# Kernel optimization log

Measured on AMD Instinct MI355X. Metric: run time of the kernel, lower is better.

The kernel has to match this reference:

```python
import jax, jax.numpy as jnp
import numpy as np

NEG_SLOPE = 0.2


def gat_layer(x, W, att_src, att_dst, bias, src, dst, N):
    # x: [N, Din], W: [Din, H*C], att_src/att_dst: [H, C], bias: [H*C]
    H, C = att_src.shape
    h = (x @ W).reshape(N, H, C)                       # [N, H, C]
    a_s = jnp.einsum('nhc,hc->nh', h, att_src)          # [N, H]
    a_d = jnp.einsum('nhc,hc->nh', h, att_dst)          # [N, H]
    e = jax.nn.leaky_relu(a_s[src] + a_d[dst], NEG_SLOPE)  # [E, H]
    # segment softmax over incoming edges of each destination node
    m = jax.ops.segment_max(e, dst, num_segments=N)     # [N, H]
    p = jnp.exp(e - m[dst])                             # [E, H]
    denom = jax.ops.segment_sum(p, dst, num_segments=N)  # [N, H]
    alpha = p / denom[dst]                              # [E, H]
    msg = alpha[:, :, None] * h[src]                    # [E, H, C]
    out = jax.ops.segment_sum(msg, dst, num_segments=N)  # [N, H, C]
    return out.reshape(N, H * C) + bias


def setup_inputs() -> dict:
    key = jax.random.key(0)
    N, E, D, H, C = 50000, 1600000, 128, 4, 32
    ks = jax.random.split(key, 12)
    x = jax.random.normal(ks[0], (N, D), dtype=jnp.float32)
    edge_index = jax.random.randint(ks[1], (2, E), 0, N, dtype=jnp.int64)
    s1 = 1.0 / np.sqrt(D)
    W1 = jax.random.normal(ks[2], (D, H * C), dtype=jnp.float32) * s1
    att_src1 = jax.random.normal(ks[3], (H, C), dtype=jnp.float32) * (1.0 / np.sqrt(C))
    att_dst1 = jax.random.normal(ks[4], (H, C), dtype=jnp.float32) * (1.0 / np.sqrt(C))
    bias1 = jnp.zeros((H * C,), dtype=jnp.float32)
    s2 = 1.0 / np.sqrt(H * C)
    W2 = jax.random.normal(ks[5], (H * C, 1), dtype=jnp.float32) * s2
    att_src2 = jax.random.normal(ks[6], (1, 1), dtype=jnp.float32)
    att_dst2 = jax.random.normal(ks[7], (1, 1), dtype=jnp.float32)
    bias2 = jnp.zeros((1,), dtype=jnp.float32)
    return {
        'x': x, 'edge_index': edge_index,
        'W1': W1, 'att_src1': att_src1, 'att_dst1': att_dst1, 'bias1': bias1,
        'W2': W2, 'att_src2': att_src2, 'att_dst2': att_dst2, 'bias2': bias2,
    }


def reference(x, edge_index, W1, att_src1, att_dst1, bias1, W2, att_src2, att_dst2, bias2):
    N = x.shape[0]
    # PyG GATConv default: add self-loops
    loop = jnp.arange(N, dtype=edge_index.dtype)
    src = jnp.concatenate([edge_index[0], loop])
    dst = jnp.concatenate([edge_index[1], loop])
    # dropout(p=0.5) is identity in eval mode
    h = gat_layer(x, W1, att_src1, att_dst1, bias1, src, dst, N)   # [N, H*C]
    h = jax.nn.elu(h)
    out = gat_layer(h, W2, att_src2, att_dst2, bias2, src, dst, N)  # [N, 1]
    return out.squeeze(-1)  # [N]
```

## Files before the change

### kernel.cpp

```cpp
#include <hip/hip_runtime.h>
#include <hip/hip_fp16.h>
#include <stdint.h>

#define NEG_SLOPE 0.2f
#define BSHIFT 7
#define NB 256

__device__ __forceinline__ float lrelu(float x){ return x > 0.f ? x : NEG_SLOPE * x; }
__device__ __forceinline__ float elu1(float x){ return x > 0.f ? x : expm1f(x); }
__device__ __forceinline__ unsigned fenc(float f){
  unsigned u = __float_as_uint(f);
  return (u & 0x80000000u) ? ~u : (u | 0x80000000u);
}
__device__ __forceinline__ float fdec(unsigned u){
  return (u & 0x80000000u) ? __uint_as_float(u & 0x7fffffffu) : __uint_as_float(~u);
}

__global__ __launch_bounds__(256) void k_gemm1(
    const float* __restrict__ x, const float* __restrict__ W1,
    const float* __restrict__ atts, const float* __restrict__ attd,
    __half* __restrict__ h1, float* __restrict__ as1, float* __restrict__ ad1,
    float* __restrict__ gblkmax, int N){
  __shared__ float xs[128 * 128];
  int n0 = blockIdx.x * 128;
  int t = threadIdx.x;
  {
    int row = t & 127;
    int kc = t >> 7;
    int n = n0 + row;
    const float4* x4 = (const float4*)x;
    #pragma unroll 4
    for (int i = 0; i < 16; ++i){
      float4 v = (n < N) ? x4[(size_t)n * 32 + kc * 16 + i]
                         : make_float4(0.f, 0.f, 0.f, 0.f);
      int k = kc * 64 + 4 * i;
      xs[(k + 0) * 128 + row] = v.x;
      xs[(k + 1) * 128 + row] = v.y;
      xs[(k + 2) * 128 + row] = v.z;
      xs[(k + 3) * 128 + row] = v.w;
    }
  }
  __syncthreads();
  int m = t & 15;
  int rg = t >> 4;
  int rb = rg * 8;
  const float4* W14 = (const float4*)W1;
  float acc[8][8];
  #pragma unroll
  for (int r = 0; r < 8; ++r)
    #pragma unroll
    for (int c = 0; c < 8; ++c) acc[r][c] = 0.f;
  #pragma unroll 2
  for (int k = 0; k < 128; ++k){
    float4 w0 = W14[k * 32 + 2 * m];
    float4 w1 = W14[k * 32 + 2 * m + 1];
    float4 xa = *(const float4*)&xs[k * 128 + rb];
    float4 xb = *(const float4*)&xs[k * 128 + rb + 4];
    float xr[8] = {xa.x, xa.y, xa.z, xa.w, xb.x, xb.y, xb.z, xb.w};
    float wc[8] = {w0.x, w0.y, w0.z, w0.w, w1.x, w1.y, w1.z, w1.w};
    #pragma unroll
    for (int r = 0; r < 8; ++r)
      #pragma unroll
      for (int c = 0; c < 8; ++c)
        acc[r][c] = fmaf(xr[r], wc[c], acc[r][c]);
  }
  float4 av0 = ((const float4*)atts)[2 * m], av1 = ((const float4*)atts)[2 * m + 1];
  float4 dv0 = ((const float4*)attd)[2 * m], dv1 = ((const float4*)attd)[2 * m + 1];
  int h = m >> 2;
  float lmax = -INFINITY;
  #pragma unroll
  for (int r = 0; r < 8; ++r){
    int n = n0 + rb + r;
    if (n < N){
      union { __half2 hh[4]; float4 f; } u;
      u.hh[0] = __floats2half2_rn(acc[r][0], acc[r][1]);
      u.hh[1] = __floats2half2_rn(acc[r][2], acc[r][3]);
      u.hh[2] = __floats2half2_rn(acc[r][4], acc[r][5]);
      u.hh[3] = __floats2half2_rn(acc[r][6], acc[r][7]);
      *(float4*)(h1 + (size_t)n * 128 + 8 * m) = u.f;
    }
    float s  = acc[r][0]*av0.x + acc[r][1]*av0.y + acc[r][2]*av0.z + acc[r][3]*av0.w
             + acc[r][4]*av1.x + acc[r][5]*av1.y + acc[r][6]*av1.z + acc[r][7]*av1.w;
    float dd = acc[r][0]*dv0.x + acc[r][1]*dv0.y + acc[r][2]*dv0.z + acc[r][3]*dv0.w
             + acc[r][4]*dv1.x + acc[r][5]*dv1.y + acc[r][6]*dv1.z + acc[r][7]*dv1.w;
    s  += __shfl_down(s, 1);  s  += __shfl_down(s, 2);
    dd += __shfl_down(dd, 1); dd += __shfl_down(dd, 2);
    lmax = fmaxf(lmax, s);
    if ((m & 3) == 0 && n < N){
      as1[n * 4 + h] = s;
      ad1[n * 4 + h] = dd;
    }
  }
  __syncthreads();
  if ((m & 3) == 0) xs[(m >> 2) * 16 + rg] = lmax;
  __syncthreads();
  if (t < 4){
    float mx = xs[t * 16];
    #pragma unroll
    for (int i = 1; i < 16; ++i) mx = fmaxf(mx, xs[t * 16 + i]);
    gblkmax[blockIdx.x * 4 + t] = mx;
  }
}


__global__ void k_bhist(const int* __restrict__ ei, int* __restrict__ gcnt,
                        int E, int N, int B, int chunk){
  __shared__ int hist[512];
  for (int t = threadIdx.x; t < B; t += 256) hist[t] = 0;
  __syncthreads();
  int T = E + N;
  int lo = blockIdx.x * chunk;
  int hi = min(lo + chunk, T);
  for (int i = lo + (int)threadIdx.x; i < hi; i += 256){
    int d = (i < E) ? ei[E + i] : (i - E);
    atomicAdd(&hist[d >> BSHIFT], 1);
  }
  __syncthreads();
  for (int t = threadIdx.x; t < B; t += 256) gcnt[blockIdx.x * B + t] = hist[t];
}

__global__ void k_bprefix(const int* __restrict__ gcnt, int* __restrict__ ecur,
                          int* __restrict__ btot, int B){
  int b = blockIdx.x;
  int t = threadIdx.x;
  int v = gcnt[t * B + b];
  int lane = t & 63, wid = t >> 6;
  int x = v;
  #pragma unroll
  for (int off = 1; off < 64; off <<= 1){
    int tmp = __shfl_up(x, off, 64);
    if (lane >= off) x += tmp;
  }
  __shared__ int ws[4];
  if (lane == 63) ws[wid] = x;
  __syncthreads();
  if (t == 0){
    int s = 0;
    #pragma unroll
    for (int i = 0; i < 4; ++i){ int tmp = ws[i]; ws[i] = s; s += tmp; }
  }
  __syncthreads();
  int excl = ws[wid] + x - v;
  ecur[b * NB + t] = excl;
  if (t == 255) btot[b] = excl + v;
}

__global__ void k_btscan(const int* __restrict__ btot, int* __restrict__ bstart,
                         const float* __restrict__ gblkmax, float* __restrict__ asmaxf,
                         unsigned* __restrict__ h2mm, int B, int T){
  __shared__ int wsum[16];
  __shared__ int carry_s;
  __shared__ unsigned smenc[4];
  int lane = threadIdx.x & 63, wid = threadIdx.x >> 6;
  if (threadIdx.x == 0) carry_s = 0;
  if (threadIdx.x < 4) smenc[threadIdx.x] = 0u;
  __syncthreads();
  for (int base = 0; base < B; base += 1024){
    int i = base + (int)threadIdx.x;
    int v = (i < B) ? btot[i] : 0;
    int x = v;
    #pragma unroll
    for (int off = 1; off < 64; off <<= 1){
      int t = __shfl_up(x, off, 64);
      if (lane >= off) x += t;
    }
    if (lane == 63) wsum[wid] = x;
    __syncthreads();
    if (wid == 0 && lane < 16){
      int w = wsum[lane];
      #pragma unroll
      for (int off = 1; off < 16; off <<= 1){
        int t = __shfl_up(w, off, 64);
        if (lane >= off) w += t;
      }
      wsum[lane] = w;
    }
    __syncthreads();
    int carry = carry_s;
    int prefix = carry + (wid ? wsum[wid - 1] : 0);
    if (i < B) bstart[i] = prefix + x - v;
    __syncthreads();
    if (threadIdx.x == 1023) carry_s = carry + wsum[15];
    __syncthreads();
  }
  if (threadIdx.x == 0) bstart[B] = T;
  float lmax = -INFINITY;
  for (int i = threadIdx.x; i < B * 4; i += 1024) lmax = fmaxf(lmax, gblkmax[i]);
  atomicMax(&smenc[threadIdx.x & 3], fenc(lmax));
  __syncthreads();
  if (threadIdx.x < 4) asmaxf[threadIdx.x] = fdec(smenc[threadIdx.x]);
  if (threadIdx.x < 2) h2mm[threadIdx.x] = 0u;
}

__global__ void k_bscatter(const int* __restrict__ ei, const int* __restrict__ ecur,
                           const int* __restrict__ bstart,
                           unsigned* __restrict__ ebuf,
                           int E, int N, int B, int chunk){
  __shared__ int cur[512];
  for (int t = threadIdx.x; t < B; t += 256)
    cur[t] = ecur[t * NB + blockIdx.x] + bstart[t];
  __syncthreads();
  int T = E + N;
  int lo = blockIdx.x * chunk;
  int hi = min(lo + chunk, T);
  for (int i = lo + (int)threadIdx.x; i < hi; i += 256){
    int s, d;
    if (i < E){ s = ei[i]; d = ei[E + i]; } else { s = d = i - E; }
    int pos = atomicAdd(&cur[d >> BSHIFT], 1);
    ebuf[pos] = ((unsigned)(d & 127) << 25) | (unsigned)s;
  }
}

__global__ void k_bfinal(const unsigned* __restrict__ ebuf,
                         const int* __restrict__ bstart,
                         int* __restrict__ csr, int* __restrict__ rs,
                         int N, int B, int T){
  int b = blockIdx.x;
  int d0 = b << BSHIFT;
  int dcount = min(128, N - d0);
  int ebeg = bstart[b];
  int eend = bstart[b + 1];
  __shared__ int hist[128];
  __shared__ int excl[128];
  if (threadIdx.x < 128) hist[threadIdx.x] = 0;
  __syncthreads();
  for (int i = ebeg + (int)threadIdx.x; i < eend; i += 256)
    atomicAdd(&hist[ebuf[i] >> 25], 1);
  __syncthreads();
  if (threadIdx.x < 64){
    int l = threadIdx.x;
    int v0 = hist[l], v1 = hist[l + 64];
    int s0 = v0, s1 = v1;
    #pragma unroll
    for (int off = 1; off < 64; off <<= 1){
      int t0 = __shfl_up(s0, off, 64); if (l >= off) s0 += t0;
      int t1 = __shfl_up(s1, off, 64); if (l >= off) s1 += t1;
    }
    int tot0 = __shfl(s0, 63, 64);
    excl[l] = s0 - v0;
    excl[l + 64] = tot0 + s1 - v1;
  }
  __syncthreads();
  if (threadIdx.x < dcount) rs[d0 + threadIdx.x] = ebeg + excl[threadIdx.x];
  if (threadIdx.x < 128) hist[threadIdx.x] = excl[threadIdx.x];
  if (b == 0 && threadIdx.x == 255) rs[N] = T;
  __syncthreads();
  for (int i = ebeg + (int)threadIdx.x; i < eend; i += 256){
    unsigned e = ebuf[i];
    int pos = ebeg + atomicAdd(&hist[e >> 25], 1);
    csr[pos] = (int)(e & 0x01FFFFFFu);
  }
}

__global__ void k_agg1(const int* __restrict__ csr, const int* __restrict__ rs,
                       const float* __restrict__ as1, const float* __restrict__ ad1,
                       const float* __restrict__ asmaxf,
                       const float4* __restrict__ h1,
                       const float* __restrict__ bias1,
                       const float* __restrict__ W2, float* __restrict__ h2, int N){
  int wv = threadIdx.x >> 6;
  int lane = threadIdx.x & 63;
  int d = blockIdx.x * 4 + wv;
  if (d >= N) return;
  int g = lane >> 4;
  int m = lane & 15;
  int h = m >> 2;
  float adh = ad1[d * 4 + h];
  float M = lrelu(asmaxf[h] + adh);
  int beg = rs[d], end = rs[d + 1];
  float den = 0.f;
  float a0=0.f,a1=0.f,a2=0.f,a3=0.f,a4=0.f,a5=0.f,a6=0.f,a7=0.f;
  int j = beg;
  for (; j + 8 <= end; j += 8){
    int sA = csr[j + g];
    int sB = csr[j + 4 + g];
    float eA = lrelu(as1[sA * 4 + h] + adh);
    float eB = lrelu(as1[sB * 4 + h] + adh);
    float pA = __expf(eA - M);
    float pB = __expf(eB - M);
    float4 rA = h1[(size_t)sA * 16 + m];
    float4 rB = h1[(size_t)sB * 16 + m];
    den += pA + pB;
    float2 cA0 = __half22float2(*(__half2*)&rA.x);
    float2 cA1 = __half22float2(*(__half2*)&rA.y);
    float2 cA2 = __half22float2(*(__half2*)&rA.z);
    float2 cA3 = __half22float2(*(__half2*)&rA.w);
    a0 = fmaf(pA, cA0.x, a0); a1 = fmaf(pA, cA0.y, a1);
    a2 = fmaf(pA, cA1.x, a2); a3 = fmaf(pA, cA1.y, a3);
    a4 = fmaf(pA, cA2.x, a4); a5 = fmaf(pA, cA2.y, a5);
    a6 = fmaf(pA, cA3.x, a6); a7 = fmaf(pA, cA3.y, a7);
    float2 cB0 = __half22float2(*(__half2*)&rB.x);
    float2 cB1 = __half22float2(*(__half2*)&rB.y);
    float2 cB2 = __half22float2(*(__half2*)&rB.z);
    float2 cB3 = __half22float2(*(__half2*)&rB.w);
    a0 = fmaf(pB, cB0.x, a0); a1 = fmaf(pB, cB0.y, a1);
    a2 = fmaf(pB, cB1.x, a2); a3 = fmaf(pB, cB1.y, a3);
    a4 = fmaf(pB, cB2.x, a4); a5 = fmaf(pB, cB2.y, a5);
    a6 = fmaf(pB, cB3.x, a6); a7 = fmaf(pB, cB3.y, a7);
  }
  for (; j < end; j += 4){
    int slot = j + g;
    bool v = slot < end;
    int s = csr[v ? slot : beg];
    float e = lrelu(as1[s * 4 + h] + adh);
    float p = v ? __expf(e - M) : 0.f;
    float4 raw = h1[(size_t)s * 16 + m];
    float2 c0 = __half22float2(*(__half2*)&raw.x);
    float2 c1 = __half22float2(*(__half2*)&raw.y);
    float2 c2 = __half22float2(*(__half2*)&raw.z);
    float2 c3 = __half22float2(*(__half2*)&raw.w);
    den += p;
    a0 = fmaf(p, c0.x, a0); a1 = fmaf(p, c0.y, a1);
    a2 = fmaf(p, c1.x, a2); a3 = fmaf(p, c1.y, a3);
    a4 = fmaf(p, c2.x, a4); a5 = fmaf(p, c2.y, a5);
    a6 = fmaf(p, c3.x, a6); a7 = fmaf(p, c3.y, a7);
  }
  #define CMB(v) v += __shfl_xor(v, 16); v += __shfl_xor(v, 32);
  CMB(a0) CMB(a1) CMB(a2) CMB(a3) CMB(a4) CMB(a5) CMB(a6) CMB(a7) CMB(den)
  #undef CMB
  float part = 0.f;
  if (lane < 16){
    float invden = 1.f / den;
    float4 b03 = ((const float4*)bias1)[2 * m];
    float4 b47 = ((const float4*)bias1)[2 * m + 1];
    float4 w03 = ((const float4*)W2)[2 * m];
    float4 w47 = ((const float4*)W2)[2 * m + 1];
    part  = elu1(a0 * invden + b03.x) * w03.x;
    part += elu1(a1 * invden + b03.y) * w03.y;
    part += elu1(a2 * invden + b03.z) * w03.z;
    part += elu1(a3 * invden + b03.w) * w03.w;
    part += elu1(a4 * invden + b47.x) * w47.x;
    part += elu1(a5 * invden + b47.y) * w47.y;
    part += elu1(a6 * invden + b47.z) * w47.z;
    part += elu1(a7 * invden + b47.w) * w47.w;
  }
  #pragma unroll
  for (int off = 8; off; off >>= 1) part += __shfl_down(part, off);
  if (lane == 0) h2[d] = part;
}

__global__ void k_h2mm(const float* __restrict__ h2, unsigned* __restrict__ h2mm, int N){
  float mx = -INFINITY, mn = INFINITY;
  for (int i = blockIdx.x * blockDim.x + threadIdx.x; i < N; i += gridDim.x * blockDim.x){
    float v = h2[i];
    mx = fmaxf(mx, v); mn = fminf(mn, v);
  }
  #pragma unroll
  for (int off = 1; off < 64; off <<= 1){
    mx = fmaxf(mx, __shfl_xor(mx, off));
    mn = fminf(mn, __shfl_xor(mn, off));
  }
  if ((threadIdx.x & 63) == 0){
    atomicMax(&h2mm[0], fenc(mx));
    atomicMax(&h2mm[1], fenc(-mn));
  }
}

__global__ void k_agg2(const int* __restrict__ csr, const int* __restrict__ rs,
                       const float* __restrict__ h2, const unsigned* __restrict__ h2mm,
                       const float* __restrict__ as2p, const float* __restrict__ ad2p,
                       const float* __restrict__ bias2, float* __restrict__ out, int N){
  int wv = threadIdx.x >> 6;
  int lane = threadIdx.x & 63;
  int d = blockIdx.x * 4 + wv;
  if (d >= N) return;
  float asc = as2p[0];
  float hmax = fdec(h2mm[0]), hmn = -fdec(h2mm[1]);
  float bound = (asc >= 0.f) ? asc * hmax : asc * hmn;
  float hd = h2[d] * ad2p[0];
  float M = lrelu(bound + hd);
  int beg = rs[d], end = rs[d + 1];
  float den = 0.f, acc = 0.f;
  for (int j = beg + lane; j < end; j += 64){
    float hs = h2[csr[j]];
    float p = __expf(lrelu(hs * asc + hd) - M);
    den += p;
    acc = fmaf(p, hs, acc);
  }
  #pragma unroll
  for (int off = 32; off; off >>= 1){
    den += __shfl_xor(den, off);
    acc += __shfl_xor(acc, off);
  }
  if (lane == 0) out[d] = acc / den + bias2[0];
}

extern "C" void kernel_launch(void* const* d_in, const int* in_sizes, int n_in,
                              void* d_out, int out_size, void* d_ws, size_t ws_size,
                              hipStream_t stream){
  const float* x     = (const float*)d_in[0];
  const int*   ei    = (const int*)  d_in[1];
  const float* W1    = (const float*)d_in[2];
  const float* atts1 = (const float*)d_in[3];
  const float* attd1 = (const float*)d_in[4];
  const float* bias1 = (const float*)d_in[5];
  const float* W2    = (const float*)d_in[6];
  const float* atts2 = (const float*)d_in[7];
  const float* attd2 = (const float*)d_in[8];
  const float* bias2 = (const float*)d_in[9];

  int N = in_sizes[0] / 128;
  int E = in_sizes[1] / 2;
  int T = E + N;
  int B = (N + 127) >> BSHIFT;
  int chunk = (T + NB - 1) / NB;

  uintptr_t base = (uintptr_t)d_ws;
  auto take = [&](size_t bytes) -> uintptr_t {
    base = (base + 255) & ~(uintptr_t)255;
    uintptr_t r = base;
    base += bytes;
    return r;
  };
  __half* h1     = (__half*)  take((size_t)N * 128 * 2);
  unsigned* ebuf = (unsigned*)take((size_t)T * 4);
  float*  as1    = (float*)   take((size_t)N * 4 * 4);
  float*  ad1    = (float*)   take((size_t)N * 4 * 4);
  float*  h2     = (float*)   take((size_t)N * 4);
  int*    gcnt   = (int*)     take((size_t)NB * B * 4);
  int*    ecur   = (int*)     take((size_t)NB * B * 4);
  int*    csr    = (int*)     take((size_t)T * 4);
  int*    rs     = (int*)     take((size_t)(N + 1) * 4);
  int*    btot   = (int*)     take((size_t)B * 4);
  int*    bstart = (int*)     take((size_t)(B + 1) * 4);
  float*  gblkmax= (float*)   take((size_t)((N + 127) / 128) * 4 * 4);
  float*  asmaxf = (float*)   take(4 * 4);
  unsigned* h2mm = (unsigned*)take(2 * 4);

  k_gemm1   <<<(N + 127) / 128, 256, 0, stream>>>(x, W1, atts1, attd1, h1, as1, ad1,
                                                  gblkmax, N);
  k_bhist   <<<NB, 256, 0, stream>>>(ei, gcnt, E, N, B, chunk);
  k_bprefix <<<B, 256, 0, stream>>>(gcnt, ecur, btot, B);
  k_btscan  <<<1, 1024, 0, stream>>>(btot, bstart, gblkmax, asmaxf, h2mm, B, T);
  k_bscatter<<<NB, 256, 0, stream>>>(ei, ecur, bstart, ebuf, E, N, B, chunk);
  k_bfinal  <<<B, 256, 0, stream>>>(ebuf, bstart, csr, rs, N, B, T);
  k_agg1    <<<(N + 3) / 4, 256, 0, stream>>>(csr, rs, as1, ad1, asmaxf,
                                              (const float4*)h1, bias1, W2, h2, N);
  k_h2mm    <<<64, 256, 0, stream>>>(h2, h2mm, N);
  k_agg2    <<<(N + 3) / 4, 256, 0, stream>>>(csr, rs, h2, h2mm, atts2, attd2,
                                              bias2, (float*)d_out, N);
}
```

Measured before the change: 168.8 us.

## Fuse histogram into GEMM launch, fold h2 min/max into agg1, narrow agg2 groups

The bucket histogram is merged into the GEMM kernel as extra blocks, so the two independent stages share one launch and can overlap. The separate h2 min/max reduction kernel is removed: each agg1 block reduces its four outputs and issues atomics directly. agg2 now assigns 16 lanes per destination node instead of a full 64-lane wavefront, which suits an average degree of about 33. The costs are roughly 12.5k extra global atomics from agg1 and a heavier LDS footprint on the histogram blocks, since they now inherit the GEMM's 64KB shared array.

```diff
diff --git a/kernel.cpp b/kernel.cpp
--- a/kernel.cpp
+++ b/kernel.cpp
@@ -16,12 +16,30 @@
   return (u & 0x80000000u) ? __uint_as_float(u & 0x7fffffffu) : __uint_as_float(~u);
 }
 
-__global__ __launch_bounds__(256) void k_gemm1(
+__global__ __launch_bounds__(256) void k_gemm1_hist(
     const float* __restrict__ x, const float* __restrict__ W1,
     const float* __restrict__ atts, const float* __restrict__ attd,
     __half* __restrict__ h1, float* __restrict__ as1, float* __restrict__ ad1,
-    float* __restrict__ gblkmax, int N){
+    float* __restrict__ gblkmax,
+    const int* __restrict__ ei, int* __restrict__ gcnt,
+    int E, int N, int B, int chunk, int G){
   __shared__ float xs[128 * 128];
+  if (blockIdx.x >= G){
+    int bid = blockIdx.x - G;
+    int* hist = (int*)xs;
+    for (int t = threadIdx.x; t < B; t += 256) hist[t] = 0;
+    __syncthreads();
+    int T = E + N;
+    int lo = bid * chunk;
+    int hi = min(lo + chunk, T);
+    for (int i = lo + (int)threadIdx.x; i < hi; i += 256){
+      int d = (i < E) ? ei[E + i] : (i - E);
+      atomicAdd(&hist[d >> BSHIFT], 1);
+    }
+    __syncthreads();
+    for (int t = threadIdx.x; t < B; t += 256) gcnt[bid * B + t] = hist[t];
+    return;
+  }
   int n0 = blockIdx.x * 128;
   int t = threadIdx.x;
   {
@@ -102,23 +120,6 @@
   }
 }
 
-
-__global__ void k_bhist(const int* __restrict__ ei, int* __restrict__ gcnt,
-                        int E, int N, int B, int chunk){
-  __shared__ int hist[512];
-  for (int t = threadIdx.x; t < B; t += 256) hist[t] = 0;
-  __syncthreads();
-  int T = E + N;
-  int lo = blockIdx.x * chunk;
-  int hi = min(lo + chunk, T);
-  for (int i = lo + (int)threadIdx.x; i < hi; i += 256){
-    int d = (i < E) ? ei[E + i] : (i - E);
-    atomicAdd(&hist[d >> BSHIFT], 1);
-  }
-  __syncthreads();
-  for (int t = threadIdx.x; t < B; t += 256) gcnt[blockIdx.x * B + t] = hist[t];
-}
-
 __global__ void k_bprefix(const int* __restrict__ gcnt, int* __restrict__ ecur,
                           int* __restrict__ btot, int B){
   int b = blockIdx.x;
@@ -257,17 +258,20 @@
                        const float* __restrict__ asmaxf,
                        const float4* __restrict__ h1,
                        const float* __restrict__ bias1,
-                       const float* __restrict__ W2, float* __restrict__ h2, int N){
+                       const float* __restrict__ W2, float* __restrict__ h2,
+                       unsigned* __restrict__ h2mm, int N){
+  __shared__ float hmax4[4], hmin4[4];
   int wv = threadIdx.x >> 6;
   int lane = threadIdx.x & 63;
   int d = blockIdx.x * 4 + wv;
-  if (d >= N) return;
+  bool valid = d < N;
   int g = lane >> 4;
   int m = lane & 15;
   int h = m >> 2;
-  float adh = ad1[d * 4 + h];
+  float adh = valid ? ad1[d * 4 + h] : 0.f;
   float M = lrelu(asmaxf[h] + adh);
-  int beg = rs[d], end = rs[d + 1];
+  int beg = 0, end = 0;
+  if (valid){ beg = rs[d]; end = rs[d + 1]; }
   float den = 0.f;
   float a0=0.f,a1=0.f,a2=0.f,a3=0.f,a4=0.f,a5=0.f,a6=0.f,a7=0.f;
   int j = beg;
@@ -336,21 +340,15 @@
   }
   #pragma unroll
   for (int off = 8; off; off >>= 1) part += __shfl_down(part, off);
-  if (lane == 0) h2[d] = part;
-}
-
-__global__ void k_h2mm(const float* __restrict__ h2, unsigned* __restrict__ h2mm, int N){
-  float mx = -INFINITY, mn = INFINITY;
-  for (int i = blockIdx.x * blockDim.x + threadIdx.x; i < N; i += gridDim.x * blockDim.x){
-    float v = h2[i];
-    mx = fmaxf(mx, v); mn = fminf(mn, v);
-  }
-  #pragma unroll
-  for (int off = 1; off < 64; off <<= 1){
-    mx = fmaxf(mx, __shfl_xor(mx, off));
-    mn = fminf(mn, __shfl_xor(mn, off));
-  }
-  if ((threadIdx.x & 63) == 0){
+  if (lane == 0){
+    if (valid) h2[d] = part;
+    hmax4[wv] = valid ? part : -INFINITY;
+    hmin4[wv] = valid ? part : INFINITY;
+  }
+  __syncthreads();
+  if (threadIdx.x == 0){
+    float mx = fmaxf(fmaxf(hmax4[0], hmax4[1]), fmaxf(hmax4[2], hmax4[3]));
+    float mn = fminf(fminf(hmin4[0], hmin4[1]), fminf(hmin4[2], hmin4[3]));
     atomicMax(&h2mm[0], fenc(mx));
     atomicMax(&h2mm[1], fenc(-mn));
   }
@@ -360,9 +358,9 @@
                        const float* __restrict__ h2, const unsigned* __restrict__ h2mm,
                        const float* __restrict__ as2p, const float* __restrict__ ad2p,
                        const float* __restrict__ bias2, float* __restrict__ out, int N){
-  int wv = threadIdx.x >> 6;
-  int lane = threadIdx.x & 63;
-  int d = blockIdx.x * 4 + wv;
+  int grp = threadIdx.x >> 4;
+  int l16 = threadIdx.x & 15;
+  int d = blockIdx.x * 16 + grp;
   if (d >= N) return;
   float asc = as2p[0];
   float hmax = fdec(h2mm[0]), hmn = -fdec(h2mm[1]);
@@ -371,18 +369,18 @@
   float M = lrelu(bound + hd);
   int beg = rs[d], end = rs[d + 1];
   float den = 0.f, acc = 0.f;
-  for (int j = beg + lane; j < end; j += 64){
+  for (int j = beg + l16; j < end; j += 16){
     float hs = h2[csr[j]];
     float p = __expf(lrelu(hs * asc + hd) - M);
     den += p;
     acc = fmaf(p, hs, acc);
   }
   #pragma unroll
-  for (int off = 32; off; off >>= 1){
-    den += __shfl_xor(den, off);
-    acc += __shfl_xor(acc, off);
-  }
-  if (lane == 0) out[d] = acc / den + bias2[0];
+  for (int off = 8; off; off >>= 1){
+    den += __shfl_xor(den, off, 16);
+    acc += __shfl_xor(acc, off, 16);
+  }
+  if (l16 == 0) out[d] = acc / den + bias2[0];
 }
 
 extern "C" void kernel_launch(void* const* d_in, const int* in_sizes, int n_in,
@@ -404,6 +402,7 @@
   int T = E + N;
   int B = (N + 127) >> BSHIFT;
   int chunk = (T + NB - 1) / NB;
+  int G = (N + 127) / 128;
 
   uintptr_t base = (uintptr_t)d_ws;
   auto take = [&](size_t bytes) -> uintptr_t {
@@ -423,20 +422,18 @@
   int*    rs     = (int*)     take((size_t)(N + 1) * 4);
   int*    btot   = (int*)     take((size_t)B * 4);
   int*    bstart = (int*)     take((size_t)(B + 1) * 4);
-  float*  gblkmax= (float*)   take((size_t)((N + 127) / 128) * 4 * 4);
+  float*  gblkmax= (float*)   take((size_t)G * 4 * 4);
   float*  asmaxf = (float*)   take(4 * 4);
   unsigned* h2mm = (unsigned*)take(2 * 4);
 
-  k_gemm1   <<<(N + 127) / 128, 256, 0, stream>>>(x, W1, atts1, attd1, h1, as1, ad1,
-                                                  gblkmax, N);
-  k_bhist   <<<NB, 256, 0, stream>>>(ei, gcnt, E, N, B, chunk);
+  k_gemm1_hist<<<G + NB, 256, 0, stream>>>(x, W1, atts1, attd1, h1, as1, ad1,
+                                           gblkmax, ei, gcnt, E, N, B, chunk, G);
   k_bprefix <<<B, 256, 0, stream>>>(gcnt, ecur, btot, B);
   k_btscan  <<<1, 1024, 0, stream>>>(btot, bstart, gblkmax, asmaxf, h2mm, B, T);
   k_bscatter<<<NB, 256, 0, stream>>>(ei, ecur, bstart, ebuf, E, N, B, chunk);
   k_bfinal  <<<B, 256, 0, stream>>>(ebuf, bstart, csr, rs, N, B, T);
   k_agg1    <<<(N + 3) / 4, 256, 0, stream>>>(csr, rs, as1, ad1, asmaxf,
-                                              (const float4*)h1, bias1, W2, h2, N);
-  k_h2mm    <<<64, 256, 0, stream>>>(h2, h2mm, N);
-  k_agg2    <<<(N + 3) / 4, 256, 0, stream>>>(csr, rs, h2, h2mm, atts2, attd2,
-                                              bias2, (float*)d_out, N);
-}
+                                              (const float4*)h1, bias1, W2, h2, h2mm, N);
+  k_agg2    <<<(N + 15) / 16, 256, 0, stream>>>(csr, rs, h2, h2mm, atts2, attd2,
+                                                bias2, (float*)d_out, N);
+}
```

After: 401.3 us. 138% more time.
